# Optimization experiments

Hardware: AMD Instinct MI355X
Metric: run time of the kernel (lower is better)

Reference implementation:

```python
import jax, jax.numpy as jnp
import numpy as np

N_FFT = 2048
HOP = 512
BATCH = 16
LENGTH = 262144


def _fourier_kernels(n_fft):
    # freq_scale='no': bin k uses frequency k; hann window, fftbins=True
    s = np.arange(n_fft, dtype=np.float64)
    win = 0.5 - 0.5 * np.cos(2.0 * np.pi * s / n_fft)
    phase = 2.0 * np.pi * s[:, None] * s[None, :] / n_fft  # (k, n)
    wsin = (win[None, :] * np.sin(phase)).astype(np.float32)[:, None, :]  # (n_fft,1,n_fft)
    wcos = (win[None, :] * np.cos(phase)).astype(np.float32)[:, None, :]
    return wsin, wcos


def setup_inputs() -> dict:
    key = jax.random.key(0)
    x = jax.random.normal(key, (BATCH, LENGTH), dtype=jnp.float32)
    wsin_np, wcos_np = _fourier_kernels(N_FFT)
    return {"x": x, "wsin": jnp.asarray(wsin_np), "wcos": jnp.asarray(wcos_np)}


def reference(x, wsin, wcos):
    # broadcast (batch, len) -> (batch, 1, len)
    x = x[:, None, :]
    # center=True, pad_mode='reflect': pad n_fft//2 on both sides
    x = jnp.pad(x, ((0, 0), (0, 0), (N_FFT // 2, N_FFT // 2)), mode="reflect")
    dn = ("NCH", "OIH", "NCH")
    imag = jax.lax.conv_general_dilated(x, wsin, (HOP,), "VALID", dimension_numbers=dn)
    real = jax.lax.conv_general_dilated(x, wcos, (HOP,), "VALID", dimension_numbers=dn)
    return (real, -imag)  # each (batch, n_fft, frames)
```

## Files before the change

kernel.cpp:

```cpp
#include <hip/hip_runtime.h>
#include <stdint.h>
#include <math.h>


#define N_FFT   2048
#define HOP     512
#define BATCH   16
#define LENGTH  262144
#define FRAMES  513
#define OHALF   ((size_t)BATCH * N_FFT * FRAMES)
#define KS      1026
#define PAIRS   257

#define XW(w) ((w) ^ (((w) >> 4) & 15))

#define TWO_PI_OVER_N  3.0679615757712823e-3f

__device__ __forceinline__ float2 cmul(float2 a, float2 w) {
    return make_float2(a.x * w.x - a.y * w.y, a.x * w.y + a.y * w.x);
}
__device__ __forceinline__ float2 csq(float2 w) {
    return make_float2(w.x * w.x - w.y * w.y, 2.f * w.x * w.y);
}


__global__ __launch_bounds__(256, 5) void fft_pairs(
    const float* __restrict__ x, float2* __restrict__ sc)
{
    __shared__ float2 buf[2][2048];

    const int tid = threadIdx.x;
    const int p   = blockIdx.x;
    const int b   = blockIdx.y;
    const int fA  = 2 * p;
    const int fB  = 2 * p + 1;
    const bool hasB = (fB < FRAMES);
    const float* xb = x + (size_t)b * LENGTH;
    const bool interior = (p >= 1 && p <= 254);

    {
        const int baseA = fA * HOP - (N_FFT / 2);
        const int baseB = fB * HOP - (N_FFT / 2);
        #pragma unroll
        for (int u = 0; u < 2; ++u) {
            int idx = tid + 256 * u;
            float sn, cs;
            __sincosf((float)idx * TWO_PI_OVER_N, &sn, &cs);
            float w0 = 0.5f - 0.5f * cs;
            float w1v = 0.5f + 0.5f * sn;
            float w2v = 0.5f + 0.5f * cs;
            float w3v = 0.5f - 0.5f * sn;

            float xa0, xa1, xa2, xa3, xb0, xb1, xb2, xb3;
            if (interior) {
                xa0 = xb[baseA + idx];
                xa1 = xb[baseA + idx + 512];
                xa2 = xb[baseA + idx + 1024];
                xa3 = xb[baseA + idx + 1536];
                xb0 = xa1;
                xb1 = xa2;
                xb2 = xa3;
                xb3 = xb[baseB + idx + 1536];
            } else {
                #pragma unroll
                for (int m = 0; m < 4; ++m) {
                    int ja = baseA + idx + 512 * m;
                    ja = (ja < 0) ? -ja : ((ja >= LENGTH) ? 2 * LENGTH - 2 - ja : ja);
                    float va = xb[ja];
                    float vb = 0.f;
                    if (hasB) {
                        int jb = baseB + idx + 512 * m;
                        jb = (jb < 0) ? -jb : ((jb >= LENGTH) ? 2 * LENGTH - 2 - jb : jb);
                        vb = xb[jb];
                    }
                    if (m == 0) { xa0 = va; xb0 = vb; }
                    else if (m == 1) { xa1 = va; xb1 = vb; }
                    else if (m == 2) { xa2 = va; xb2 = vb; }
                    else { xa3 = va; xb3 = vb; }
                }
            }

            float2 a0 = make_float2(xa0 * w0, xb0 * w0);
            float2 a1 = make_float2(xa1 * w1v, xb1 * w1v);
            float2 a2 = make_float2(xa2 * w2v, xb2 * w2v);
            float2 a3 = make_float2(xa3 * w3v, xb3 * w3v);

            float2 t0 = make_float2(a0.x + a2.x, a0.y + a2.y);
            float2 t1 = make_float2(a0.x - a2.x, a0.y - a2.y);
            float2 t2 = make_float2(a1.x + a3.x, a1.y + a3.y);
            float2 t3 = make_float2(a1.x - a3.x, a1.y - a3.y);
            float2 y0 = make_float2(t0.x + t2.x, t0.y + t2.y);
            float2 y1 = make_float2(t1.x + t3.y, t1.y - t3.x);
            float2 y2 = make_float2(t0.x - t2.x, t0.y - t2.y);
            float2 y3 = make_float2(t1.x - t3.y, t1.y + t3.x);

            float2 tw1 = make_float2(cs, -sn);
            float2 tw2 = csq(tw1);
            float2 tw3 = cmul(tw1, tw2);

            int o = 4 * idx;
            buf[0][XW(o)]     = y0;
            buf[0][XW(o + 1)] = cmul(y1, tw1);
            buf[0][XW(o + 2)] = cmul(y2, tw2);
            buf[0][XW(o + 3)] = cmul(y3, tw3);
        }
    }
    __syncthreads();

    int src = 0;
    #pragma unroll
    for (int ls = 1; ls < 5; ++ls) {
        const int s  = 1 << (2 * ls);
        const float2* X = buf[src];
        float2*       Y = buf[src ^ 1];
        #pragma unroll
        for (int u = 0; u < 2; ++u) {
            int idx = tid + 256 * u;
            int sp  = idx & ~(s - 1);
            int wi  = XW(idx);
            float2 a0 = X[wi];
            float2 a1 = X[wi + 512];
            float2 a2 = X[wi + 1024];
            float2 a3 = X[wi + 1536];

            float sn, cs;
            __sincosf((float)sp * TWO_PI_OVER_N, &sn, &cs);
            float2 w1 = make_float2(cs, -sn);
            float2 w2 = csq(w1);
            float2 w3 = cmul(w1, w2);

            float2 t0 = make_float2(a0.x + a2.x, a0.y + a2.y);
            float2 t1 = make_float2(a0.x - a2.x, a0.y - a2.y);
            float2 t2 = make_float2(a1.x + a3.x, a1.y + a3.y);
            float2 t3 = make_float2(a1.x - a3.x, a1.y - a3.y);
            float2 y0 = make_float2(t0.x + t2.x, t0.y + t2.y);
            float2 y1 = make_float2(t1.x + t3.y, t1.y - t3.x);
            float2 y2 = make_float2(t0.x - t2.x, t0.y - t2.y);
            float2 y3 = make_float2(t1.x - t3.y, t1.y + t3.x);

            int o = idx + 3 * sp;
            Y[XW(o)]         = y0;
            Y[XW(o + s)]     = cmul(y1, w1);
            Y[XW(o + 2 * s)] = cmul(y2, w2);
            Y[XW(o + 3 * s)] = cmul(y3, w3);
        }
        __syncthreads();
        src ^= 1;
    }

    const float2* X5 = buf[src];
    float2* scA = sc + ((size_t)b * FRAMES + fA) * KS;
    float2* scB = sc + ((size_t)b * FRAMES + fB) * KS;
    #pragma unroll
    for (int j = 0; j < 5; ++j) {
        int k = tid + 256 * j;
        if (k <= 1024) {
            int m2 = (2048 - k) & 2047;
            float2 u0, u1, v0, v1;
            if (k < 1024) {
                int wa = XW(k);
                u0 = X5[wa]; u1 = X5[wa + 1024];
                u0 = make_float2(u0.x + u1.x, u0.y + u1.y);
            } else {
                u0 = X5[0]; u1 = X5[1024];
                u0 = make_float2(u0.x - u1.x, u0.y - u1.y);
            }
            if (m2 < 1024) {
                int wa = XW(m2);
                v0 = X5[wa]; v1 = X5[wa + 1024];
                v0 = make_float2(v0.x + v1.x, v0.y + v1.y);
            } else {
                int wa = XW(m2 - 1024);
                v0 = X5[wa]; v1 = X5[wa + 1024];
                v0 = make_float2(v0.x - v1.x, v0.y - v1.y);
            }
            float2 A = make_float2(0.5f * (u0.x + v0.x), 0.5f * (u0.y - v0.y));
            float2 B = make_float2(0.5f * (u0.y + v0.y), 0.5f * (v0.x - u0.x));
            scA[k] = A;
            if (hasB) scB[k] = B;
        }
    }
}

__global__ __launch_bounds__(256, 5) void transpose_out(
    const float2* __restrict__ sc, float* __restrict__ out)
{
    __shared__ float tile[2][64][64];

    const int b  = blockIdx.x;
    const int kt = blockIdx.y;
    const int ft = blockIdx.z;
    const int k0 = kt * 64;
    const int f0 = ft * 64;
    const int tid = threadIdx.x;

    #pragma unroll
    for (int i = 0; i < 16; ++i) {
        int idx = tid + 256 * i;
        int fl = idx >> 6, kl = idx & 63;
        int f = f0 + fl, k = k0 + kl;
        float2 v = make_float2(0.f, 0.f);
        if (f < FRAMES && k <= 1024)
            v = sc[((size_t)b * FRAMES + f) * KS + k];
        tile[0][fl][kl ^ fl] = v.x;
        tile[1][fl][kl ^ fl] = v.y;
    }
    __syncthreads();

    const int wave = tid >> 6, lane = tid & 63;
    const int t = f0 + lane;
    const bool tok = (t < FRAMES);
    float* o0 = out + (size_t)b * ((size_t)N_FFT * FRAMES);
    float* o1 = out + OHALF + (size_t)b * ((size_t)N_FFT * FRAMES);

    for (int kl = wave; kl < 64; kl += 4) {
        int k = k0 + kl;
        if (k > 1024) continue;
        float vr = tile[0][lane][kl ^ lane];
        float vi = tile[1][lane][kl ^ lane];
        if (tok) {
            o0[(size_t)k * FRAMES + t] = vr;
            o1[(size_t)k * FRAMES + t] = vi;
            if (k >= 1 && k <= 1023) {
                o0[(size_t)(N_FFT - k) * FRAMES + t] = vr;
                o1[(size_t)(N_FFT - k) * FRAMES + t] = -vi;
            }
        }
    }
}


__global__ void dft_naive(const float* __restrict__ x,
                          const float* __restrict__ wsin,
                          const float* __restrict__ wcos,
                          float* __restrict__ out)
{
    size_t i = (size_t)blockIdx.x * 256 + threadIdx.x;
    if (i >= OHALF) return;
    int t = (int)(i % FRAMES);
    size_t r = i / FRAMES;
    int k = (int)(r % N_FFT);
    int b = (int)(r / N_FFT);
    float sr = 0.f, si = 0.f;
    int base = t * HOP - N_FFT / 2;
    for (int n = 0; n < N_FFT; ++n) {
        int j = base + n;
        j = (j < 0) ? -j : ((j >= LENGTH) ? (2 * LENGTH - 2 - j) : j);
        float xv = x[(size_t)b * LENGTH + j];
        sr += xv * wcos[(size_t)k * N_FFT + n];
        si += xv * wsin[(size_t)k * N_FFT + n];
    }
    out[i] = sr;
    out[OHALF + i] = -si;
}


extern "C" void kernel_launch(void* const* d_in, const int* in_sizes, int n_in,
                              void* d_out, int out_size, void* d_ws, size_t ws_size,
                              hipStream_t stream) {
    const float* x    = (const float*)d_in[0];
    const float* wsin = (const float*)d_in[1];
    const float* wcos = (const float*)d_in[2];
    float* out = (float*)d_out;

    const size_t sc_f2   = (size_t)BATCH * FRAMES * KS;
    const size_t need_ft = sc_f2 * sizeof(float2);
    if (ws_size >= need_ft) {
        float2* sc = (float2*)d_ws;
        fft_pairs<<<dim3(PAIRS, BATCH), 256, 0, stream>>>(x, sc);
        transpose_out<<<dim3(BATCH, 17, 9), 256, 0, stream>>>(sc, out);
        return;
    }

    dft_naive<<<(int)((OHALF + 255) / 256), 256, 0, stream>>>(x, wsin, wcos, out);
}
```

Baseline: 246.0 us.

## Switch FFT to radix-8 stages with final radix-4 pass

Restructures the 2048-point FFT from five radix-4 stages plus a split final radix-2 into three radix-8 stages followed by one untwiddled radix-4 stage. The goal is fewer shared-memory round trips, fewer __syncthreads barriers and fewer twiddle sincos evaluations per frame pair. The pack/unpack step reads the completed spectrum directly instead of folding the last radix-2 in. The cost is more live registers per thread (8 complex values plus twiddles), which could lower occupancy under launch_bounds(256,5).

```diff
diff --git a/kernel.cpp b/kernel.cpp
--- a/kernel.cpp
+++ b/kernel.cpp
@@ -15,12 +15,76 @@
 #define XW(w) ((w) ^ (((w) >> 4) & 15))
 
 #define TWO_PI_OVER_N  3.0679615757712823e-3f
+#define RSQRT2         0.70710678118654752f
 
 __device__ __forceinline__ float2 cmul(float2 a, float2 w) {
     return make_float2(a.x * w.x - a.y * w.y, a.x * w.y + a.y * w.x);
 }
 __device__ __forceinline__ float2 csq(float2 w) {
     return make_float2(w.x * w.x - w.y * w.y, 2.f * w.x * w.y);
+}
+
+__device__ __forceinline__ void dft4(float2 z0, float2 z1, float2 z2, float2 z3,
+                                     float2& y0, float2& y1, float2& y2, float2& y3)
+{
+    float2 t0 = make_float2(z0.x + z2.x, z0.y + z2.y);
+    float2 t1 = make_float2(z0.x - z2.x, z0.y - z2.y);
+    float2 t2 = make_float2(z1.x + z3.x, z1.y + z3.y);
+    float2 t3 = make_float2(z1.x - z3.x, z1.y - z3.y);
+    y0 = make_float2(t0.x + t2.x, t0.y + t2.y);
+    y1 = make_float2(t1.x + t3.y, t1.y - t3.x);
+    y2 = make_float2(t0.x - t2.x, t0.y - t2.y);
+    y3 = make_float2(t1.x - t3.y, t1.y + t3.x);
+}
+
+__device__ __forceinline__ void r8_store(float2* __restrict__ Y, const float2 a[8],
+                                         float2 w1, int obase, int s)
+{
+    float2 u0 = make_float2(a[0].x + a[4].x, a[0].y + a[4].y);
+    float2 u1 = make_float2(a[1].x + a[5].x, a[1].y + a[5].y);
+    float2 u2 = make_float2(a[2].x + a[6].x, a[2].y + a[6].y);
+    float2 u3 = make_float2(a[3].x + a[7].x, a[3].y + a[7].y);
+    float2 v0 = make_float2(a[0].x - a[4].x, a[0].y - a[4].y);
+    float2 v1 = make_float2(a[1].x - a[5].x, a[1].y - a[5].y);
+    float2 v2 = make_float2(a[2].x - a[6].x, a[2].y - a[6].y);
+    float2 v3 = make_float2(a[3].x - a[7].x, a[3].y - a[7].y);
+    v1 = make_float2(RSQRT2 * (v1.x + v1.y), RSQRT2 * (v1.y - v1.x));
+    v2 = make_float2(v2.y, -v2.x);
+    v3 = make_float2(RSQRT2 * (v3.y - v3.x), -RSQRT2 * (v3.x + v3.y));
+
+    float2 E0, E1, E2, E3, O0, O1, O2, O3;
+    dft4(u0, u1, u2, u3, E0, E1, E2, E3);
+    dft4(v0, v1, v2, v3, O0, O1, O2, O3);
+
+    float2 w2 = csq(w1);
+    float2 w3 = cmul(w1, w2);
+    float2 w4 = csq(w2);
+    float2 w5 = cmul(w2, w3);
+    float2 w6 = csq(w3);
+    float2 w7 = cmul(w3, w4);
+
+    Y[XW(obase)]         = E0;
+    Y[XW(obase + s)]     = cmul(O0, w1);
+    Y[XW(obase + 2 * s)] = cmul(E1, w2);
+    Y[XW(obase + 3 * s)] = cmul(O1, w3);
+    Y[XW(obase + 4 * s)] = cmul(E2, w4);
+    Y[XW(obase + 5 * s)] = cmul(O2, w5);
+    Y[XW(obase + 6 * s)] = cmul(E3, w6);
+    Y[XW(obase + 7 * s)] = cmul(O3, w7);
+}
+
+template<int S>
+__device__ __forceinline__ void r8_stage(const float2* __restrict__ X,
+                                         float2* __restrict__ Y, int idx)
+{
+    float2 a[8];
+    const int wi = XW(idx);
+    #pragma unroll
+    for (int m = 0; m < 8; ++m) a[m] = X[wi + 256 * m];
+    const int sp = idx & ~(S - 1);
+    float sn, cs;
+    __sincosf((float)sp * TWO_PI_OVER_N, &sn, &cs);
+    r8_store(Y, a, make_float2(cs, -sn), idx + 7 * sp, S);
 }
 
 
@@ -40,115 +104,73 @@
 
     {
         const int baseA = fA * HOP - (N_FFT / 2);
-        const int baseB = fB * HOP - (N_FFT / 2);
+        float xa[8], xv[8];
+        if (interior) {
+            #pragma unroll
+            for (int m = 0; m < 8; ++m) xa[m] = xb[baseA + tid + 256 * m];
+            #pragma unroll
+            for (int m = 0; m < 6; ++m) xv[m] = xa[m + 2];
+            xv[6] = xb[baseA + 512 + tid + 256 * 6];
+            xv[7] = xb[baseA + 512 + tid + 256 * 7];
+        } else {
+            const int baseB = baseA + 512;
+            #pragma unroll
+            for (int m = 0; m < 8; ++m) {
+                int ja = baseA + tid + 256 * m;
+                ja = (ja < 0) ? -ja : ((ja >= LENGTH) ? 2 * LENGTH - 2 - ja : ja);
+                xa[m] = xb[ja];
+                float vb = 0.f;
+                if (hasB) {
+                    int jb = baseB + tid + 256 * m;
+                    jb = (jb < 0) ? -jb : ((jb >= LENGTH) ? 2 * LENGTH - 2 - jb : jb);
+                    vb = xb[jb];
+                }
+                xv[m] = vb;
+            }
+        }
+        float sn, cs;
+        __sincosf((float)tid * TWO_PI_OVER_N, &sn, &cs);
+        const float cd = RSQRT2 * (cs - sn);
+        const float cp = RSQRT2 * (cs + sn);
+        float wv[8];
+        wv[0] = 0.5f - 0.5f * cs;  wv[1] = 0.5f - 0.5f * cd;
+        wv[2] = 0.5f + 0.5f * sn;  wv[3] = 0.5f + 0.5f * cp;
+        wv[4] = 0.5f + 0.5f * cs;  wv[5] = 0.5f + 0.5f * cd;
+        wv[6] = 0.5f - 0.5f * sn;  wv[7] = 0.5f - 0.5f * cp;
+
+        float2 a[8];
+        #pragma unroll
+        for (int m = 0; m < 8; ++m)
+            a[m] = make_float2(xa[m] * wv[m], xv[m] * wv[m]);
+
+        r8_store(buf[0], a, make_float2(cs, -sn), 8 * tid, 1);
+    }
+    __syncthreads();
+
+    r8_stage<8>(buf[0], buf[1], tid);
+    __syncthreads();
+
+    r8_stage<64>(buf[1], buf[0], tid);
+    __syncthreads();
+
+    {
+        const float2* X = buf[0];
+        float2*       Y = buf[1];
         #pragma unroll
         for (int u = 0; u < 2; ++u) {
             int idx = tid + 256 * u;
-            float sn, cs;
-            __sincosf((float)idx * TWO_PI_OVER_N, &sn, &cs);
-            float w0 = 0.5f - 0.5f * cs;
-            float w1v = 0.5f + 0.5f * sn;
-            float w2v = 0.5f + 0.5f * cs;
-            float w3v = 0.5f - 0.5f * sn;
-
-            float xa0, xa1, xa2, xa3, xb0, xb1, xb2, xb3;
-            if (interior) {
-                xa0 = xb[baseA + idx];
-                xa1 = xb[baseA + idx + 512];
-                xa2 = xb[baseA + idx + 1024];
-                xa3 = xb[baseA + idx + 1536];
-                xb0 = xa1;
-                xb1 = xa2;
-                xb2 = xa3;
-                xb3 = xb[baseB + idx + 1536];
-            } else {
-                #pragma unroll
-                for (int m = 0; m < 4; ++m) {
-                    int ja = baseA + idx + 512 * m;
-                    ja = (ja < 0) ? -ja : ((ja >= LENGTH) ? 2 * LENGTH - 2 - ja : ja);
-                    float va = xb[ja];
-                    float vb = 0.f;
-                    if (hasB) {
-                        int jb = baseB + idx + 512 * m;
-                        jb = (jb < 0) ? -jb : ((jb >= LENGTH) ? 2 * LENGTH - 2 - jb : jb);
-                        vb = xb[jb];
-                    }
-                    if (m == 0) { xa0 = va; xb0 = vb; }
-                    else if (m == 1) { xa1 = va; xb1 = vb; }
-                    else if (m == 2) { xa2 = va; xb2 = vb; }
-                    else { xa3 = va; xb3 = vb; }
-                }
-            }
-
-            float2 a0 = make_float2(xa0 * w0, xb0 * w0);
-            float2 a1 = make_float2(xa1 * w1v, xb1 * w1v);
-            float2 a2 = make_float2(xa2 * w2v, xb2 * w2v);
-            float2 a3 = make_float2(xa3 * w3v, xb3 * w3v);
-
-            float2 t0 = make_float2(a0.x + a2.x, a0.y + a2.y);
-            float2 t1 = make_float2(a0.x - a2.x, a0.y - a2.y);
-            float2 t2 = make_float2(a1.x + a3.x, a1.y + a3.y);
-            float2 t3 = make_float2(a1.x - a3.x, a1.y - a3.y);
-            float2 y0 = make_float2(t0.x + t2.x, t0.y + t2.y);
-            float2 y1 = make_float2(t1.x + t3.y, t1.y - t3.x);
-            float2 y2 = make_float2(t0.x - t2.x, t0.y - t2.y);
-            float2 y3 = make_float2(t1.x - t3.y, t1.y + t3.x);
-
-            float2 tw1 = make_float2(cs, -sn);
-            float2 tw2 = csq(tw1);
-            float2 tw3 = cmul(tw1, tw2);
-
-            int o = 4 * idx;
-            buf[0][XW(o)]     = y0;
-            buf[0][XW(o + 1)] = cmul(y1, tw1);
-            buf[0][XW(o + 2)] = cmul(y2, tw2);
-            buf[0][XW(o + 3)] = cmul(y3, tw3);
-        }
-    }
-    __syncthreads();
-
-    int src = 0;
-    #pragma unroll
-    for (int ls = 1; ls < 5; ++ls) {
-        const int s  = 1 << (2 * ls);
-        const float2* X = buf[src];
-        float2*       Y = buf[src ^ 1];
-        #pragma unroll
-        for (int u = 0; u < 2; ++u) {
-            int idx = tid + 256 * u;
-            int sp  = idx & ~(s - 1);
             int wi  = XW(idx);
-            float2 a0 = X[wi];
-            float2 a1 = X[wi + 512];
-            float2 a2 = X[wi + 1024];
-            float2 a3 = X[wi + 1536];
-
-            float sn, cs;
-            __sincosf((float)sp * TWO_PI_OVER_N, &sn, &cs);
-            float2 w1 = make_float2(cs, -sn);
-            float2 w2 = csq(w1);
-            float2 w3 = cmul(w1, w2);
-
-            float2 t0 = make_float2(a0.x + a2.x, a0.y + a2.y);
-            float2 t1 = make_float2(a0.x - a2.x, a0.y - a2.y);
-            float2 t2 = make_float2(a1.x + a3.x, a1.y + a3.y);
-            float2 t3 = make_float2(a1.x - a3.x, a1.y - a3.y);
-            float2 y0 = make_float2(t0.x + t2.x, t0.y + t2.y);
-            float2 y1 = make_float2(t1.x + t3.y, t1.y - t3.x);
-            float2 y2 = make_float2(t0.x - t2.x, t0.y - t2.y);
-            float2 y3 = make_float2(t1.x - t3.y, t1.y + t3.x);
-
-            int o = idx + 3 * sp;
-            Y[XW(o)]         = y0;
-            Y[XW(o + s)]     = cmul(y1, w1);
-            Y[XW(o + 2 * s)] = cmul(y2, w2);
-            Y[XW(o + 3 * s)] = cmul(y3, w3);
-        }
-        __syncthreads();
-        src ^= 1;
-    }
-
-    const float2* X5 = buf[src];
+            float2 y0, y1, y2, y3;
+            dft4(X[wi], X[wi + 512], X[wi + 1024], X[wi + 1536], y0, y1, y2, y3);
+            Y[wi]        = y0;
+            Y[wi + 512]  = y1;
+            Y[wi + 1024] = y2;
+            Y[wi + 1536] = y3;
+        }
+    }
+    __syncthreads();
+
+    const float2* X5 = buf[1];
     float2* scA = sc + ((size_t)b * FRAMES + fA) * KS;
     float2* scB = sc + ((size_t)b * FRAMES + fB) * KS;
     #pragma unroll
@@ -156,26 +178,10 @@
         int k = tid + 256 * j;
         if (k <= 1024) {
             int m2 = (2048 - k) & 2047;
-            float2 u0, u1, v0, v1;
-            if (k < 1024) {
-                int wa = XW(k);
-                u0 = X5[wa]; u1 = X5[wa + 1024];
-                u0 = make_float2(u0.x + u1.x, u0.y + u1.y);
-            } else {
-                u0 = X5[0]; u1 = X5[1024];
-                u0 = make_float2(u0.x - u1.x, u0.y - u1.y);
-            }
-            if (m2 < 1024) {
-                int wa = XW(m2);
-                v0 = X5[wa]; v1 = X5[wa + 1024];
-                v0 = make_float2(v0.x + v1.x, v0.y + v1.y);
-            } else {
-                int wa = XW(m2 - 1024);
-                v0 = X5[wa]; v1 = X5[wa + 1024];
-                v0 = make_float2(v0.x - v1.x, v0.y - v1.y);
-            }
-            float2 A = make_float2(0.5f * (u0.x + v0.x), 0.5f * (u0.y - v0.y));
-            float2 B = make_float2(0.5f * (u0.y + v0.y), 0.5f * (v0.x - u0.x));
+            float2 zk = X5[XW(k)];
+            float2 zm = X5[XW(m2)];
+            float2 A = make_float2(0.5f * (zk.x + zm.x), 0.5f * (zk.y - zm.y));
+            float2 B = make_float2(0.5f * (zk.y + zm.y), 0.5f * (zm.x - zk.x));
             scA[k] = A;
             if (hasB) scB[k] = B;
         }
```

Result: faster. 241.1 us (-2.0%).
